# Kernel optimization log

Measured on AMD Instinct MI355X. Metric: run time of the kernel, lower is better.

The kernel has to match this reference:

```python
import jax, jax.numpy as jnp
import numpy as np

B, T, D_ENC, D_FEAT, D_WORD, H, V = 512, 80, 1024, 512, 512, 512, 10000


def setup_inputs() -> dict:
    key = jax.random.key(0)
    ks = jax.random.split(key, 8)
    s = 0.02
    return {
        "outputs_encoder": jax.random.normal(ks[0], (B, T, D_ENC), jnp.float32),
        "start_ids": jax.random.randint(ks[1], (B,), 0, V, jnp.int32),
        "W_proj": jax.random.normal(ks[2], (D_ENC, D_FEAT), jnp.float32) * s,
        "b_proj": jnp.zeros((D_FEAT,), jnp.float32),
        "embed_table": jax.random.normal(ks[3], (V, D_WORD), jnp.float32) * s,
        "W_ih": jax.random.normal(ks[4], (4 * H, D_FEAT + D_WORD), jnp.float32) * s,
        "W_hh": jax.random.normal(ks[5], (4 * H, H), jnp.float32) * s,
        "b_ih": jnp.zeros((4 * H,), jnp.float32),
        "b_hh": jnp.zeros((4 * H,), jnp.float32),
    }


def _lstm_cell(x, h, c, W_ih, W_hh, b_ih, b_hh):
    # torch.nn.LSTMCell gate order: i, f, g, o
    gates = x @ W_ih.T + b_ih + h @ W_hh.T + b_hh  # [B, 4H]
    i, f, g, o = jnp.split(gates, 4, axis=-1)
    c_new = jax.nn.sigmoid(f) * c + jax.nn.sigmoid(i) * jnp.tanh(g)
    h_new = jax.nn.sigmoid(o) * jnp.tanh(c_new)
    return h_new, c_new


def reference(outputs_encoder, start_ids, W_proj, b_proj, embed_table, W_ih, W_hh, b_ih, b_hh):
    # project encoder features: [B, T, D_FEAT]
    feats = jnp.einsum("btd,df->btf", outputs_encoder, W_proj) + b_proj
    word = embed_table[start_ids]  # [B, D_WORD] (<start> embedding, reused each step)
    h0 = jnp.zeros((feats.shape[0], W_hh.shape[1]), feats.dtype)
    c0 = jnp.zeros_like(h0)

    def step(carry, feat_t):
        h, c = carry
        x = jnp.concatenate([feat_t, word], axis=1)  # [B, D_FEAT+D_WORD]
        h, c = _lstm_cell(x, h, c, W_ih, W_hh, b_ih, b_hh)
        return (h, c), h

    (_, _), hs = jax.lax.scan(step, (h0, c0), jnp.swapaxes(feats, 0, 1))  # hs: [T, B, H]
    return jnp.swapaxes(hs, 0, 1)  # [B, T, H]
```

## Files before the change

### kernel.cpp

```cpp
#include <hip/hip_runtime.h>
#include <stdint.h>

typedef __bf16 bf16x8 __attribute__((ext_vector_type(8)));
typedef float  f32x4  __attribute__((ext_vector_type(4)));
typedef unsigned int u32x4 __attribute__((ext_vector_type(4)));
typedef unsigned long long u64;

__device__ __forceinline__ uint16_t f2b(float f) {
  uint32_t u = __float_as_uint(f);
  return (uint16_t)((u + 0x7FFFu + ((u >> 16) & 1u)) >> 16);
}
__device__ __forceinline__ float b2f(uint16_t h) {
  return __uint_as_float(((uint32_t)h) << 16);
}
__device__ __forceinline__ uint4 pack8f(float4 a, float4 b) {
  uint4 r;
  r.x = (uint32_t)f2b(a.x) | ((uint32_t)f2b(a.y) << 16);
  r.y = (uint32_t)f2b(a.z) | ((uint32_t)f2b(a.w) << 16);
  r.z = (uint32_t)f2b(b.x) | ((uint32_t)f2b(b.y) << 16);
  r.w = (uint32_t)f2b(b.z) | ((uint32_t)f2b(b.w) << 16);
  return r;
}
__device__ __forceinline__ float fsig(float x) {
  return 1.f / (1.f + __expf(-x));
}
__device__ __forceinline__ float ftanh(float x) {
  return 1.f - 2.f / (1.f + __expf(2.f * x));
}

__global__ void detect_kernel(const uint32_t* __restrict__ wproj, int* flag) {
  __shared__ int cnt;
  if (threadIdx.x == 0) cnt = 0;
  __syncthreads();
  int local = 0;
  for (int i = threadIdx.x; i < 1024; i += 256) {
    float v = __uint_as_float((wproj[i] & 0xFFFFu) << 16);
    float av = fabsf(v);
    if (av > 1e-4f && av < 0.5f) local++;
  }
  atomicAdd(&cnt, local);
  __syncthreads();
  if (threadIdx.x == 0) flag[0] = (cnt > 512) ? 1 : 0;
}

__global__ void convert_kernel(const void* __restrict__ src,
                               uint16_t* __restrict__ dst,
                               const int* __restrict__ flagp) {
  int i = blockIdx.x * 256 + threadIdx.x;
  if (*flagp) {
    ((uint4*)dst)[i] = ((const uint4*)src)[i];
  } else {
    const float* s = (const float*)src + (size_t)i * 8;
    ((uint4*)dst)[i] = pack8f(*(const float4*)s, *(const float4*)(s + 4));
  }
}

__global__ void word_kernel(const int* __restrict__ ids,
                            const void* __restrict__ embed,
                            uint16_t* __restrict__ word,
                            const int* __restrict__ flagp) {
  int c = blockIdx.x * 256 + threadIdx.x;
  int b = c >> 6, off = c & 63;
  size_t row = (size_t)ids[b] * 512;
  if (*flagp) {
    ((uint4*)word)[c] = ((const uint4*)((const uint16_t*)embed + row))[off];
  } else {
    const float* s = (const float*)embed + row + (size_t)off * 8;
    ((uint4*)word)[c] = pack8f(*(const float4*)s, *(const float4*)(s + 4));
  }
}

__global__ void bias2_kernel(const void* __restrict__ bih,
                             const void* __restrict__ bhh,
                             const void* __restrict__ bproj,
                             const uint16_t* __restrict__ Wihb,
                             float* __restrict__ bias2,
                             const int* __restrict__ flagp) {
  int j = blockIdx.x * 256 + threadIdx.x;
  int fl = *flagp;
  float s;
  if (fl) s = b2f(((const uint16_t*)bih)[j]) + b2f(((const uint16_t*)bhh)[j]);
  else    s = ((const float*)bih)[j] + ((const float*)bhh)[j];
  const uint16_t* wrow = Wihb + (size_t)j * 1024;
  float acc = 0.f;
  for (int f = 0; f < 512; f++) {
    float bp = fl ? b2f(((const uint16_t*)bproj)[f]) : ((const float*)bproj)[f];
    acc += bp * b2f(wrow[f]);
  }
  bias2[j] = s + acc;
}

template <int MODE, bool APOLY>
__global__ __launch_bounds__(256, 2)
void gemm_bt(const void* __restrict__ Av, int lda,
             const uint16_t* __restrict__ Bt, int ldb,
             void* __restrict__ Cout, int ldc, int K,
             const float* __restrict__ wg,
             const int* __restrict__ flagp, int c0) {
  __shared__ __align__(16) uint16_t As[128 * 32];
  __shared__ __align__(16) uint16_t Bs[128 * 32];
  const int tid = threadIdx.x;
  const int bm = blockIdx.y * 128, bn = blockIdx.x * 128;
  const int wid = tid >> 6, lane = tid & 63;
  const int wm = (wid >> 1) * 64, wn = (wid & 1) * 64;
  const int lrow = lane & 15, quad = lane >> 4;
  const int srow = tid >> 2, scol = (tid & 3) * 8;
  const bool a_bf16 = APOLY ? (*flagp != 0) : true;

  int r0 = bm + srow, r1 = bm + 64 + srow;
  size_t gr0, gr1;
  if (MODE == 1) {
    gr0 = (size_t)(r0 >> 4) * 80 + c0 + (r0 & 15);
    gr1 = (size_t)(r1 >> 4) * 80 + c0 + (r1 & 15);
  } else {
    gr0 = r0; gr1 = r1;
  }
  f32x4 acc[4][4] = {};

  for (int kb = 0; kb < K; kb += 32) {
    uint4 a0, a1;
    if (a_bf16) {
      a0 = *(const uint4*)((const uint16_t*)Av + gr0 * lda + kb + scol);
      a1 = *(const uint4*)((const uint16_t*)Av + gr1 * lda + kb + scol);
    } else {
      const float* p0 = (const float*)Av + gr0 * lda + kb + scol;
      const float* p1 = (const float*)Av + gr1 * lda + kb + scol;
      a0 = pack8f(*(const float4*)p0, *(const float4*)(p0 + 4));
      a1 = pack8f(*(const float4*)p1, *(const float4*)(p1 + 4));
    }
    uint4 b0 = *(const uint4*)(Bt + (size_t)(bn + srow) * ldb + kb + scol);
    uint4 b1 = *(const uint4*)(Bt + (size_t)(bn + 64 + srow) * ldb + kb + scol);
    __syncthreads();
    *(uint4*)(As + srow * 32 + scol) = a0;
    *(uint4*)(As + (64 + srow) * 32 + scol) = a1;
    *(uint4*)(Bs + srow * 32 + scol) = b0;
    *(uint4*)(Bs + (64 + srow) * 32 + scol) = b1;
    __syncthreads();
    bf16x8 af[4], bfr[4];
#pragma unroll
    for (int i = 0; i < 4; i++) {
      af[i]  = *reinterpret_cast<const bf16x8*>(As + (wm + i * 16 + lrow) * 32 + quad * 8);
      bfr[i] = *reinterpret_cast<const bf16x8*>(Bs + (wn + i * 16 + lrow) * 32 + quad * 8);
    }
#pragma unroll
    for (int i = 0; i < 4; i++)
#pragma unroll
      for (int j = 0; j < 4; j++)
        acc[i][j] = __builtin_amdgcn_mfma_f32_16x16x32_bf16(af[i], bfr[j], acc[i][j], 0, 0, 0);
  }

  if constexpr (MODE == 0) {
    uint16_t* C = (uint16_t*)Cout;
#pragma unroll
    for (int i = 0; i < 4; i++) {
      int row = bm + wm + i * 16 + quad * 4;
#pragma unroll
      for (int j = 0; j < 4; j++) {
        int col = bn + wn + j * 16 + lrow;
#pragma unroll
        for (int r = 0; r < 4; r++)
          C[(size_t)(row + r) * ldc + col] = f2b(acc[i][j][r]);
      }
    }
  } else if constexpr (MODE == 2) {
    float* C = (float*)Cout;
#pragma unroll
    for (int i = 0; i < 4; i++) {
      int row = bm + wm + i * 16 + quad * 4;
#pragma unroll
      for (int j = 0; j < 4; j++) {
        int col = bn + wn + j * 16 + lrow;
        float bias = wg[col];
#pragma unroll
        for (int r = 0; r < 4; r++)
          C[(size_t)(row + r) * ldc + col] = acc[i][j][r] + bias;
      }
    }
  } else {
    float* C = (float*)Cout;
#pragma unroll
    for (int i = 0; i < 4; i++) {
#pragma unroll
      for (int r = 0; r < 4; r++) {
        int m = bm + wm + i * 16 + quad * 4 + r;
        int b = m >> 4, t0 = m & 15;
        size_t orow = (size_t)t0 * 512 + b;
#pragma unroll
        for (int j = 0; j < 4; j++) {
          int col = bn + wn + j * 16 + lrow;
          C[orow * 2048 + col] = acc[i][j][r] + wg[(size_t)b * 2048 + col];
        }
      }
    }
  }
}

__global__ __launch_bounds__(256, 1)
void lstm16_kernel(const uint16_t* __restrict__ Whhb,
                   const float* __restrict__ xg,
                   uint16_t* __restrict__ hring,
                   float* __restrict__ cst,
                   void* __restrict__ out,
                   int tbase,
                   const int* __restrict__ flagp,
                   unsigned int* __restrict__ bar) {
  __shared__ __align__(16) uint16_t Hs[32 * 512];
  __shared__ float Gs[4][32][33];

  const int tid = threadIdx.x;
  const int bid = blockIdx.x;
  const int rb = ((bid & 7) << 1) | ((bid >> 3) & 1);
  const int cb = bid >> 4;
  const int g = tid >> 6;
  const int lane = tid & 63;
  const int lrow = lane & 15, quad = lane >> 4;
  const int fl = *flagp;

  u32x4 breg[2][16];
  {
    const uint16_t* wb = Whhb + ((size_t)(g * 512 + cb * 32 + lrow) * 512) + quad * 8;
#pragma unroll
    for (int j = 0; j < 2; j++)
#pragma unroll
      for (int kk = 0; kk < 16; kk++) {
        breg[j][kk] = *reinterpret_cast<const u32x4*>(wb + (size_t)j * 16 * 512 + kk * 32);
        asm volatile("" : "+v"(breg[j][kk]));
      }
  }

  const int erow = tid >> 3;
  const int ecol = (tid & 7) * 4;
  const int gb = rb * 32 + erow;
  const int gh = cb * 32 + ecol;
  f32x4 creg = *reinterpret_cast<const f32x4*>(cst + (size_t)gb * 512 + gh);

  const int sc16 = (tid & 7) * 16;
  const int ssw = (erow & 7) << 4;
  unsigned int* cnt = bar + rb * 64;

#pragma unroll 1
  for (int s = 0; s < 16; s++) {
    const int t = tbase + s;
    const uint16_t* hin = hring + (size_t)((t + 16) % 17) * 262144;
    uint16_t* hout = hring + (size_t)(t % 17) * 262144;

    const float* xr = xg + ((size_t)s * 512 + gb) * 2048 + gh;
    f32x4 x0 = *reinterpret_cast<const f32x4*>(xr);
    f32x4 x1 = *reinterpret_cast<const f32x4*>(xr + 512);
    f32x4 x2 = *reinterpret_cast<const f32x4*>(xr + 1024);
    f32x4 x3 = *reinterpret_cast<const f32x4*>(xr + 1536);

    {
      const char* hsrc = (const char*)(hin + (size_t)gb * 512);
      char* hdst = (char*)Hs + erow * 1024;
#pragma unroll
      for (int it = 0; it < 8; it++) {
        int bc = sc16 + it * 128;
        *reinterpret_cast<uint4*>(hdst + (bc ^ ssw)) =
            *reinterpret_cast<const uint4*>(hsrc + bc);
      }
    }
    __syncthreads();

    f32x4 acc[2][2] = {};
#pragma unroll
    for (int kk = 0; kk < 16; kk++) {
      bf16x8 af[2];
#pragma unroll
      for (int i = 0; i < 2; i++) {
        int r = i * 16 + lrow;
        int bc = kk * 64 + quad * 16;
        af[i] = *reinterpret_cast<const bf16x8*>(
            (const char*)Hs + r * 1024 + (bc ^ ((r & 7) << 4)));
      }
#pragma unroll
      for (int i = 0; i < 2; i++)
#pragma unroll
        for (int j = 0; j < 2; j++)
          acc[i][j] = __builtin_amdgcn_mfma_f32_16x16x32_bf16(
              af[i], __builtin_bit_cast(bf16x8, breg[j][kk]), acc[i][j], 0, 0, 0);
    }

#pragma unroll
    for (int i = 0; i < 2; i++)
#pragma unroll
      for (int j = 0; j < 2; j++)
#pragma unroll
        for (int r = 0; r < 4; r++)
          Gs[g][i * 16 + quad * 4 + r][j * 16 + lrow] = acc[i][j][r];
    __syncthreads();

    float hnv[4];
#pragma unroll
    for (int e = 0; e < 4; e++) {
      float p_i = Gs[0][erow][ecol + e] + x0[e];
      float p_f = Gs[1][erow][ecol + e] + x1[e];
      float p_g = Gs[2][erow][ecol + e] + x2[e];
      float p_o = Gs[3][erow][ecol + e] + x3[e];
      float si = fsig(p_i);
      float sf = fsig(p_f);
      float so = fsig(p_o);
      float tg = ftanh(p_g);
      float cn = sf * creg[e] + si * tg;
      creg[e] = cn;
      hnv[e] = so * ftanh(cn);
    }
    uint2 hp;
    hp.x = (uint32_t)f2b(hnv[0]) | ((uint32_t)f2b(hnv[1]) << 16);
    hp.y = (uint32_t)f2b(hnv[2]) | ((uint32_t)f2b(hnv[3]) << 16);
    u64 hv = (u64)hp.x | ((u64)hp.y << 32);
    __hip_atomic_store((u64*)(hout + (size_t)gb * 512 + gh), hv,
                       __ATOMIC_RELAXED, __HIP_MEMORY_SCOPE_AGENT);
    size_t oi = (size_t)gb * (80 * 512) + (size_t)t * 512 + gh;
    if (fl) {
      *reinterpret_cast<uint2*>((uint16_t*)out + oi) = hp;
    } else {
      float4 ov = make_float4(hnv[0], hnv[1], hnv[2], hnv[3]);
      *reinterpret_cast<float4*>((float*)out + oi) = ov;
    }

    __syncthreads();
    if (tid == 0) {
      __hip_atomic_fetch_add(cnt, 1u, __ATOMIC_RELAXED, __HIP_MEMORY_SCOPE_AGENT);
      if (s != 15) {
        unsigned tgt = (unsigned)(t + 1) * 16u;
        while (__hip_atomic_load(cnt, __ATOMIC_RELAXED, __HIP_MEMORY_SCOPE_AGENT) < tgt)
          __builtin_amdgcn_s_sleep(1);
      }
    }
    __syncthreads();
  }

  *reinterpret_cast<f32x4*>(cst + (size_t)gb * 512 + gh) = creg;
}

extern "C" void kernel_launch(void* const* d_in, const int* in_sizes, int n_in,
                              void* d_out, int out_size, void* d_ws, size_t ws_size,
                              hipStream_t stream) {
  const void* enc   = d_in[0];
  const int*  ids   = (const int*)d_in[1];
  const void* Wproj = d_in[2];
  const void* bproj = d_in[3];
  const void* embed = d_in[4];
  const void* Wih   = d_in[5];
  const void* Whh   = d_in[6];
  const void* bih   = d_in[7];
  const void* bhh   = d_in[8];

  uint8_t* w = (uint8_t*)d_ws;
  int*      flag   = (int*)w;
  unsigned int* bar = (unsigned int*)(w + 8192);
  float*    bias2  = (float*)(w + 16384);
  float*    wgates = (float*)(w + 32768);
  uint16_t* combT  = (uint16_t*)(w + 4227072);
  uint16_t* Wihb   = (uint16_t*)(w + 8421376);
  uint16_t* Whhb   = (uint16_t*)(w + 12615680);
  uint16_t* Wprojb = (uint16_t*)(w + 14712832);
  uint16_t* word   = (uint16_t*)(w + 15761408);
  float*    cst    = (float*)(w + 17334272);
  float*    xgbuf  = (float*)(w + 18382848);
  uint16_t* hring  = (uint16_t*)(w + 85491712);

  detect_kernel<<<1, 256, 0, stream>>>((const uint32_t*)Wproj, flag);
  convert_kernel<<<1024, 256, 0, stream>>>(Wih, Wihb, flag);
  convert_kernel<<<512, 256, 0, stream>>>(Whh, Whhb, flag);
  convert_kernel<<<256, 256, 0, stream>>>(Wproj, Wprojb, flag);
  word_kernel<<<128, 256, 0, stream>>>(ids, embed, word, flag);
  bias2_kernel<<<8, 256, 0, stream>>>(bih, bhh, bproj, Wihb, bias2, flag);

  gemm_bt<0, false><<<dim3(8, 16), 256, 0, stream>>>(Wihb, 1024, Wprojb, 512,
                                                     combT, 1024, 512, nullptr, flag, 0);
  gemm_bt<2, false><<<dim3(16, 4), 256, 0, stream>>>(word, 512, Wihb + 512, 1024,
                                                     wgates, 2048, 512, bias2, flag, 0);

  (void)hipMemsetAsync(hring + (size_t)16 * 262144, 0, 524288, stream);
  (void)hipMemsetAsync(cst, 0, 512 * 512 * 4, stream);
  (void)hipMemsetAsync(bar, 0, 4096, stream);

  const uint16_t* Whhb_a = Whhb;
  const float* xg_a = xgbuf;
  uint16_t* hring_a = hring;
  float* cst_a = cst;
  void* out_a = d_out;
  const int* flag_a = flag;
  unsigned int* bar_a = bar;

  for (int c = 0; c < 5; c++) {
    gemm_bt<1, true><<<dim3(16, 64), 256, 0, stream>>>(enc, 1024, combT, 1024,
                                                       xgbuf, 2048, 1024, wgates, flag, c * 16);
    int tbase = c * 16;
    void* kargs[] = {(void*)&Whhb_a, (void*)&xg_a, (void*)&hring_a,
                     (void*)&cst_a, (void*)&out_a, (void*)&tbase, (void*)&flag_a,
                     (void*)&bar_a};
    (void)hipLaunchCooperativeKernel(lstm16_kernel, dim3(256), dim3(256), kargs,
                                     0u, stream);
  }
}
```

Baseline: 1.097 ms.

## Use direct global-to-LDS loads in GEMM, pre-convert encoder chunks, parallelize bias reduction

The GEMM tile loads now go straight from global memory into shared memory with global_load_lds, so they no longer pass through registers. Because that path cannot convert on the fly, a new convA_kernel first converts each 16-timestep encoder chunk to bf16 in a contiguous buffer before the input-gate GEMM. The bias2 kernel changes from a serial per-thread 512-element loop to a wave-per-row reduction with shuffles. The trade is an extra conversion pass and extra buffer traffic per chunk, in exchange for lower register pressure and less load latency in the GEMM.

New measurement: 958.6 us. 12.6% less time.

```diff
diff --git a/kernel.cpp b/kernel.cpp
--- a/kernel.cpp
+++ b/kernel.cpp
@@ -26,6 +26,11 @@
 }
 __device__ __forceinline__ float ftanh(float x) {
   return 1.f - 2.f / (1.f + __expf(2.f * x));
+}
+__device__ __forceinline__ void gload_lds16(const void* g, void* l) {
+  __builtin_amdgcn_global_load_lds(
+      (const __attribute__((address_space(1))) uint32_t*)g,
+      (__attribute__((address_space(3))) uint32_t*)l, 16, 0, 0);
 }
 
 __global__ void detect_kernel(const uint32_t* __restrict__ wproj, int* flag) {
@@ -52,6 +57,21 @@
   } else {
     const float* s = (const float*)src + (size_t)i * 8;
     ((uint4*)dst)[i] = pack8f(*(const float4*)s, *(const float4*)(s + 4));
+  }
+}
+
+__global__ void convA_kernel(const void* __restrict__ enc,
+                             uint16_t* __restrict__ encb,
+                             const int* __restrict__ flagp, int c0) {
+  int i = blockIdx.x * 256 + threadIdx.x;
+  int m = i >> 7, ch = i & 127;
+  int b = m >> 4, t0 = m & 15;
+  size_t src = ((size_t)b * 80 + c0 + t0) * 1024 + (size_t)ch * 8;
+  if (*flagp) {
+    ((uint4*)encb)[i] = *(const uint4*)((const uint16_t*)enc + src);
+  } else {
+    const float* s = (const float*)enc + src;
+    ((uint4*)encb)[i] = pack8f(*(const float4*)s, *(const float4*)(s + 4));
   }
 }
 
@@ -76,27 +96,46 @@
                              const uint16_t* __restrict__ Wihb,
                              float* __restrict__ bias2,
                              const int* __restrict__ flagp) {
-  int j = blockIdx.x * 256 + threadIdx.x;
-  int fl = *flagp;
-  float s;
-  if (fl) s = b2f(((const uint16_t*)bih)[j]) + b2f(((const uint16_t*)bhh)[j]);
-  else    s = ((const float*)bih)[j] + ((const float*)bhh)[j];
-  const uint16_t* wrow = Wihb + (size_t)j * 1024;
+  const int wid = threadIdx.x >> 6, lane = threadIdx.x & 63;
+  const int j = blockIdx.x * 4 + wid;
+  const int fl = *flagp;
+  uint4 wv = *(const uint4*)(Wihb + (size_t)j * 1024 + lane * 8);
+  const uint16_t wh[8] = {
+      (uint16_t)wv.x, (uint16_t)(wv.x >> 16), (uint16_t)wv.y, (uint16_t)(wv.y >> 16),
+      (uint16_t)wv.z, (uint16_t)(wv.z >> 16), (uint16_t)wv.w, (uint16_t)(wv.w >> 16)};
+  float bp[8];
+  if (fl) {
+    uint4 pv = *(const uint4*)((const uint16_t*)bproj + lane * 8);
+    const uint16_t ph[8] = {
+        (uint16_t)pv.x, (uint16_t)(pv.x >> 16), (uint16_t)pv.y, (uint16_t)(pv.y >> 16),
+        (uint16_t)pv.z, (uint16_t)(pv.z >> 16), (uint16_t)pv.w, (uint16_t)(pv.w >> 16)};
+#pragma unroll
+    for (int e = 0; e < 8; e++) bp[e] = b2f(ph[e]);
+  } else {
+    float4 p0 = ((const float4*)bproj)[lane * 2];
+    float4 p1 = ((const float4*)bproj)[lane * 2 + 1];
+    bp[0] = p0.x; bp[1] = p0.y; bp[2] = p0.z; bp[3] = p0.w;
+    bp[4] = p1.x; bp[5] = p1.y; bp[6] = p1.z; bp[7] = p1.w;
+  }
   float acc = 0.f;
-  for (int f = 0; f < 512; f++) {
-    float bp = fl ? b2f(((const uint16_t*)bproj)[f]) : ((const float*)bproj)[f];
-    acc += bp * b2f(wrow[f]);
-  }
-  bias2[j] = s + acc;
-}
-
-template <int MODE, bool APOLY>
+#pragma unroll
+  for (int e = 0; e < 8; e++) acc += bp[e] * b2f(wh[e]);
+#pragma unroll
+  for (int m = 32; m >= 1; m >>= 1) acc += __shfl_xor(acc, m, 64);
+  if (lane == 0) {
+    float s;
+    if (fl) s = b2f(((const uint16_t*)bih)[j]) + b2f(((const uint16_t*)bhh)[j]);
+    else    s = ((const float*)bih)[j] + ((const float*)bhh)[j];
+    bias2[j] = s + acc;
+  }
+}
+
+template <int MODE>
 __global__ __launch_bounds__(256, 2)
-void gemm_bt(const void* __restrict__ Av, int lda,
+void gemm_bt(const uint16_t* __restrict__ A, int lda,
              const uint16_t* __restrict__ Bt, int ldb,
              void* __restrict__ Cout, int ldc, int K,
-             const float* __restrict__ wg,
-             const int* __restrict__ flagp, int c0) {
+             const float* __restrict__ wg) {
   __shared__ __align__(16) uint16_t As[128 * 32];
   __shared__ __align__(16) uint16_t Bs[128 * 32];
   const int tid = threadIdx.x;
@@ -105,36 +144,24 @@
   const int wm = (wid >> 1) * 64, wn = (wid & 1) * 64;
   const int lrow = lane & 15, quad = lane >> 4;
   const int srow = tid >> 2, scol = (tid & 3) * 8;
-  const bool a_bf16 = APOLY ? (*flagp != 0) : true;
-
-  int r0 = bm + srow, r1 = bm + 64 + srow;
-  size_t gr0, gr1;
-  if (MODE == 1) {
-    gr0 = (size_t)(r0 >> 4) * 80 + c0 + (r0 & 15);
-    gr1 = (size_t)(r1 >> 4) * 80 + c0 + (r1 & 15);
-  } else {
-    gr0 = r0; gr1 = r1;
-  }
+
+  const uint16_t* ga0 = A + (size_t)(bm + srow) * lda + scol;
+  const uint16_t* ga1 = A + (size_t)(bm + 64 + srow) * lda + scol;
+  const uint16_t* gb0 = Bt + (size_t)(bn + srow) * ldb + scol;
+  const uint16_t* gb1 = Bt + (size_t)(bn + 64 + srow) * ldb + scol;
+  uint16_t* la0 = As + srow * 32 + scol;
+  uint16_t* la1 = As + (64 + srow) * 32 + scol;
+  uint16_t* lb0 = Bs + srow * 32 + scol;
+  uint16_t* lb1 = Bs + (64 + srow) * 32 + scol;
+
   f32x4 acc[4][4] = {};
 
   for (int kb = 0; kb < K; kb += 32) {
-    uint4 a0, a1;
-    if (a_bf16) {
-      a0 = *(const uint4*)((const uint16_t*)Av + gr0 * lda + kb + scol);
-      a1 = *(const uint4*)((const uint16_t*)Av + gr1 * lda + kb + scol);
-    } else {
-      const float* p0 = (const float*)Av + gr0 * lda + kb + scol;
-      const float* p1 = (const float*)Av + gr1 * lda + kb + scol;
-      a0 = pack8f(*(const float4*)p0, *(const float4*)(p0 + 4));
-      a1 = pack8f(*(const float4*)p1, *(const float4*)(p1 + 4));
-    }
-    uint4 b0 = *(const uint4*)(Bt + (size_t)(bn + srow) * ldb + kb + scol);
-    uint4 b1 = *(const uint4*)(Bt + (size_t)(bn + 64 + srow) * ldb + kb + scol);
-    __syncthreads();
-    *(uint4*)(As + srow * 32 + scol) = a0;
-    *(uint4*)(As + (64 + srow) * 32 + scol) = a1;
-    *(uint4*)(Bs + srow * 32 + scol) = b0;
-    *(uint4*)(Bs + (64 + srow) * 32 + scol) = b1;
+    __syncthreads();
+    gload_lds16(ga0 + kb, la0);
+    gload_lds16(ga1 + kb, la1);
+    gload_lds16(gb0 + kb, lb0);
+    gload_lds16(gb1 + kb, lb1);
     __syncthreads();
     bf16x8 af[4], bfr[4];
 #pragma unroll
@@ -360,18 +387,19 @@
   float*    cst    = (float*)(w + 17334272);
   float*    xgbuf  = (float*)(w + 18382848);
   uint16_t* hring  = (uint16_t*)(w + 85491712);
+  uint16_t* encb   = (uint16_t*)(w + 94404608);
 
   detect_kernel<<<1, 256, 0, stream>>>((const uint32_t*)Wproj, flag);
   convert_kernel<<<1024, 256, 0, stream>>>(Wih, Wihb, flag);
   convert_kernel<<<512, 256, 0, stream>>>(Whh, Whhb, flag);
   convert_kernel<<<256, 256, 0, stream>>>(Wproj, Wprojb, flag);
   word_kernel<<<128, 256, 0, stream>>>(ids, embed, word, flag);
-  bias2_kernel<<<8, 256, 0, stream>>>(bih, bhh, bproj, Wihb, bias2, flag);
-
-  gemm_bt<0, false><<<dim3(8, 16), 256, 0, stream>>>(Wihb, 1024, Wprojb, 512,
-                                                     combT, 1024, 512, nullptr, flag, 0);
-  gemm_bt<2, false><<<dim3(16, 4), 256, 0, stream>>>(word, 512, Wihb + 512, 1024,
-                                                     wgates, 2048, 512, bias2, flag, 0);
+  bias2_kernel<<<512, 256, 0, stream>>>(bih, bhh, bproj, Wihb, bias2, flag);
+
+  gemm_bt<0><<<dim3(8, 16), 256, 0, stream>>>(Wihb, 1024, Wprojb, 512,
+                                              combT, 1024, 512, nullptr);
+  gemm_bt<2><<<dim3(16, 4), 256, 0, stream>>>(word, 512, Wihb + 512, 1024,
+                                              wgates, 2048, 512, bias2);
 
   (void)hipMemsetAsync(hring + (size_t)16 * 262144, 0, 524288, stream);
   (void)hipMemsetAsync(cst, 0, 512 * 512 * 4, stream);
@@ -386,8 +414,9 @@
   unsigned int* bar_a = bar;
 
   for (int c = 0; c < 5; c++) {
-    gemm_bt<1, true><<<dim3(16, 64), 256, 0, stream>>>(enc, 1024, combT, 1024,
-                                                       xgbuf, 2048, 1024, wgates, flag, c * 16);
+    convA_kernel<<<4096, 256, 0, stream>>>(enc, encb, flag, c * 16);
+    gemm_bt<1><<<dim3(16, 64), 256, 0, stream>>>(encb, 1024, combT, 1024,
+                                                 xgbuf, 2048, 1024, wgates);
     int tbase = c * 16;
     void* kargs[] = {(void*)&Whhb_a, (void*)&xg_a, (void*)&hring_a,
                      (void*)&cst_a, (void*)&out_a, (void*)&tbase, (void*)&flag_a,
```
